# Kernel tuning notes

Measured on AMD Instinct MI355X. Metric: run time of the kernel, lower is better.

## Reference

```python
import jax, jax.numpy as jnp
import numpy as np

D_MODEL = 2048
B, T, N = 4, 2048, 512


def setup_inputs() -> dict:
    key = jax.random.key(0)
    k1, k2, k3, k4, k5 = jax.random.split(key, 5)
    x = jax.random.normal(k1, (B, T, D_MODEL), dtype=jnp.float32)
    h_stack = jax.random.normal(k2, (B, N, D_MODEL), dtype=jnp.float32)
    m_stack = jax.random.normal(k3, (B, N, D_MODEL), dtype=jnp.float32)
    m_current = jax.random.normal(k4, (B, T, D_MODEL), dtype=jnp.float32)
    # block-causal visibility: position t can see cache entry j iff j <= t*N/T
    causal_mask = jnp.arange(N)[None, :] <= (jnp.arange(T)[:, None] * N // T)
    # learned projection, torch Linear stores weight as (out, in): u = x @ W.T
    W_u = jax.random.normal(k5, (D_MODEL, D_MODEL), dtype=jnp.float32) * (1.0 / np.sqrt(D_MODEL))
    return {"x": x, "h_stack": h_stack, "m_stack": m_stack,
            "m_current": m_current, "causal_mask": causal_mask, "W_u": W_u}


def reference(x, h_stack, m_stack, m_current, causal_mask, W_u):
    D = x.shape[-1]
    n = m_stack.shape[1]
    scale = 1.0 / jnp.sqrt(jnp.asarray(D, x.dtype))
    u = jnp.einsum('btd,ed->bte', x, W_u)                      # Linear(no bias): x @ W.T
    scores_cached = jnp.einsum('btd,bnd->btn', u, m_stack) * scale
    neg_inf = jnp.asarray(-jnp.inf, scores_cached.dtype)
    scores_cached = jnp.where(causal_mask[None, :, :], scores_cached, neg_inf)
    scores_current = jnp.sum(u * m_current, axis=-1, keepdims=True) * scale  # (B,T,1)
    all_scores = jnp.concatenate([scores_cached, scores_current], axis=-1)   # (B,T,N+1)
    attn_weights = jax.nn.softmax(all_scores, axis=-1)
    gates_cached = attn_weights[:, :, :n]
    gate_current = attn_weights[:, :, n:]
    h_retrieved = jnp.einsum('btn,bnd->btd', gates_cached, h_stack)
    return h_retrieved, gate_current, attn_weights
```

## Files before the change

### kernel.cpp

```cpp
#include <hip/hip_runtime.h>

#define D_MODEL 2048
#define B_SZ 4
#define T_SZ 2048
#define N_SZ 512

typedef __bf16 bf16x8 __attribute__((ext_vector_type(8)));
typedef float f32x4 __attribute__((ext_vector_type(4)));
typedef ushort u16x8 __attribute__((ext_vector_type(8)));

__device__ __forceinline__ ushort f2bf(float f) {
  unsigned u = __float_as_uint(f);
  unsigned r = (u + 0x7fffu + ((u >> 16) & 1u)) >> 16;
  return (ushort)r;
}
__device__ __forceinline__ float bflo(unsigned w) { return __uint_as_float(w << 16); }
__device__ __forceinline__ float bfhi(unsigned w) { return __uint_as_float(w & 0xffff0000u); }

__device__ __forceinline__ void async_ld16(const ushort* g, ushort* l) {
  __builtin_amdgcn_global_load_lds(
      (const __attribute__((address_space(1))) void*)g,
      (__attribute__((address_space(3))) void*)l, 16, 0, 0);
}

__global__ __launch_bounds__(256) void conv_all(const float* __restrict__ x,
                                                const float* __restrict__ W,
                                                const float* __restrict__ ms,
                                                ushort* __restrict__ x_bf,
                                                ushort* __restrict__ W_bf,
                                                ushort* __restrict__ ms_bf) {
  const int bid = blockIdx.x;
  const float* src;
  ushort* dst;
  long blk;
  if (bid < 8192) { src = x; dst = x_bf; blk = bid; }
  else if (bid < 10240) { src = W; dst = W_bf; blk = bid - 8192; }
  else { src = ms; dst = ms_bf; blk = bid - 10240; }
  const long i = (blk * 256 + threadIdx.x) * 8;
  float4 a = *(const float4*)(src + i);
  float4 b = *(const float4*)(src + i + 4);
  u16x8 o;
  o[0] = f2bf(a.x); o[1] = f2bf(a.y); o[2] = f2bf(a.z); o[3] = f2bf(a.w);
  o[4] = f2bf(b.x); o[5] = f2bf(b.y); o[6] = f2bf(b.z); o[7] = f2bf(b.w);
  *(u16x8*)(dst + i) = o;
}

__global__ __launch_bounds__(256) void transpose_conv(const float* __restrict__ src,
                                                      ushort* __restrict__ dst) {
  __shared__ ushort tile[32][33];
  const int b = blockIdx.z;
  const int n0 = blockIdx.x * 32, d0 = blockIdx.y * 32;
  const int tx = threadIdx.x, ty = threadIdx.y;
  const float* s = src + (long)b * N_SZ * D_MODEL;
  ushort* d = dst + (long)b * D_MODEL * N_SZ;
#pragma unroll
  for (int r = 0; r < 4; r++)
    tile[ty + r * 8][tx] = f2bf(s[(long)(n0 + ty + r * 8) * D_MODEL + d0 + tx]);
  __syncthreads();
#pragma unroll
  for (int r = 0; r < 4; r++)
    d[(long)(d0 + ty + r * 8) * N_SZ + n0 + tx] = tile[tx][ty + r * 8];
}

template <int TM, int MASKMODE, bool OUT_BF16>
__global__ __launch_bounds__(256) void gemm_bt(const ushort* __restrict__ A,
                                               const ushort* __restrict__ Bt,
                                               void* __restrict__ Cv, int N, int K,
                                               long sA, long sB, long sC, float scale) {
  constexpr int NA = TM / 16;
  constexpr int NCH = NA + 8;
  constexpr int NC = NCH / 4;
  constexpr int NI = TM / 32;
  __shared__ __align__(16) ushort sa[TM * 32];
  __shared__ __align__(16) ushort sb[128 * 32];
  const int bz = blockIdx.z;
  const int row0 = blockIdx.y * TM;
  const int col0 = blockIdx.x * 128;
  if (MASKMODE == 1 && col0 > ((row0 + TM - 1) >> 2)) return;
  int Kend = K;
  if (MASKMODE == 2) {
    int kl = ((row0 + TM - 1) >> 2) + 1;
    Kend = min(K, (kl + 31) & ~31);
  }
  const ushort* Ab = A + (long)bz * sA;
  const ushort* Bb = Bt + (long)bz * sB;

  const int tid = threadIdx.x;
  const int w = tid >> 6, lane = tid & 63;
  const int wr = w >> 1, wc = w & 1;
  const int quad = lane >> 4, l16 = lane & 15;

  f32x4 acc[NI][4];
#pragma unroll
  for (int i = 0; i < NI; i++)
#pragma unroll
    for (int j = 0; j < 4; j++) acc[i][j] = (f32x4){0.f, 0.f, 0.f, 0.f};

  const int lrow = lane >> 2;
  const int lcol = (lane & 3) * 8;
  const ushort* gsrc[NC];
  ushort* ldst[NC];
#pragma unroll
  for (int t = 0; t < NC; t++) {
    const int c = w * NC + t;
    if (c < NA) {
      ldst[t] = sa + c * 512;
      gsrc[t] = Ab + (long)(row0 + c * 16 + lrow) * K + lcol;
    } else {
      ldst[t] = sb + (c - NA) * 512;
      gsrc[t] = Bb + (long)(col0 + (c - NA) * 16 + lrow) * K + lcol;
    }
  }

  for (int k0 = 0; k0 < Kend; k0 += 32) {
#pragma unroll
    for (int t = 0; t < NC; t++) async_ld16(gsrc[t] + k0, ldst[t]);
    __syncthreads();
    bf16x8 af[NI], bfr[4];
#pragma unroll
    for (int i = 0; i < NI; i++)
      af[i] = *(const bf16x8*)(sa + (wr * (TM / 2) + i * 16 + l16) * 32 + quad * 8);
#pragma unroll
    for (int j = 0; j < 4; j++)
      bfr[j] = *(const bf16x8*)(sb + (wc * 64 + j * 16 + l16) * 32 + quad * 8);
#pragma unroll
    for (int i = 0; i < NI; i++)
#pragma unroll
      for (int j = 0; j < 4; j++)
        acc[i][j] = __builtin_amdgcn_mfma_f32_16x16x32_bf16(af[i], bfr[j], acc[i][j], 0, 0, 0);
    __syncthreads();
  }

#pragma unroll
  for (int i = 0; i < NI; i++) {
    const int rb = row0 + wr * (TM / 2) + i * 16 + quad * 4;
#pragma unroll
    for (int j = 0; j < 4; j++) {
      const int c = col0 + wc * 64 + j * 16 + l16;
#pragma unroll
      for (int r = 0; r < 4; r++) {
        float v = acc[i][j][r] * scale;
        long off = (long)bz * sC + (long)(rb + r) * N + c;
        if (OUT_BF16)
          ((ushort*)Cv)[off] = f2bf(v);
        else
          ((float*)Cv)[off] = v;
      }
    }
  }
}

__global__ __launch_bounds__(256) void softmax_gate(const ushort* __restrict__ u_bf,
                                                    const float* __restrict__ m_cur,
                                                    const float* __restrict__ scores,
                                                    float* __restrict__ out_gc,
                                                    float* __restrict__ out_attn,
                                                    ushort* __restrict__ gates_bf) {
  const int wv = threadIdx.x >> 6, lane = threadIdx.x & 63;
  const int bt = blockIdx.x * 4 + wv;
  const int t = bt & (T_SZ - 1);
  const ushort* urow = u_bf + (long)bt * D_MODEL;
  const float* mrow = m_cur + (long)bt * D_MODEL;

  float part = 0.f;
#pragma unroll
  for (int c = 0; c < 4; c++) {
    uint4 uv = *(const uint4*)(urow + c * 512 + lane * 8);
    float4 m0 = *(const float4*)(mrow + c * 512 + lane * 8);
    float4 m1 = *(const float4*)(mrow + c * 512 + lane * 8 + 4);
    part += bflo(uv.x) * m0.x + bfhi(uv.x) * m0.y + bflo(uv.y) * m0.z + bfhi(uv.y) * m0.w +
            bflo(uv.z) * m1.x + bfhi(uv.z) * m1.y + bflo(uv.w) * m1.z + bfhi(uv.w) * m1.w;
  }
#pragma unroll
  for (int m = 32; m; m >>= 1) part += __shfl_xor(part, m, 64);
  const float curs = part * 0.022097086912079608f;

  const int nmax = t >> 2;
  const float* srow = scores + (long)bt * N_SZ;
  float sc[8];
  float lmax = curs;
#pragma unroll
  for (int k = 0; k < 8; k++) {
    const int n = k * 64 + lane;
    sc[k] = srow[n];
    if (n <= nmax) lmax = fmaxf(lmax, sc[k]);
  }
#pragma unroll
  for (int m = 32; m; m >>= 1) lmax = fmaxf(lmax, __shfl_xor(lmax, m, 64));

  float lsum = (lane == 0) ? __expf(curs - lmax) : 0.f;
#pragma unroll
  for (int k = 0; k < 8; k++) {
    const int n = k * 64 + lane;
    sc[k] = (n <= nmax) ? __expf(sc[k] - lmax) : 0.f;
    lsum += sc[k];
  }
#pragma unroll
  for (int m = 32; m; m >>= 1) lsum += __shfl_xor(lsum, m, 64);
  const float inv = 1.f / lsum;

  float* arow = out_attn + (long)bt * (N_SZ + 1);
  ushort* grow = gates_bf + (long)bt * N_SZ;
#pragma unroll
  for (int k = 0; k < 8; k++) {
    const int n = k * 64 + lane;
    const float wgt = sc[k] * inv;
    arow[n] = wgt;
    grow[n] = f2bf(wgt);
  }
  if (lane == 0) {
    const float g = __expf(curs - lmax) * inv;
    arow[N_SZ] = g;
    out_gc[bt] = g;
  }
}

extern "C" void kernel_launch(void* const* d_in, const int* in_sizes, int n_in,
                              void* d_out, int out_size, void* d_ws, size_t ws_size,
                              hipStream_t stream) {
  const float* x = (const float*)d_in[0];
  const float* h_stack = (const float*)d_in[1];
  const float* m_stack = (const float*)d_in[2];
  const float* m_cur = (const float*)d_in[3];
  const float* W = (const float*)d_in[5];

  float* out = (float*)d_out;
  float* out_h = out;
  float* out_gc = out + (long)B_SZ * T_SZ * D_MODEL;
  float* out_attn = out_gc + B_SZ * T_SZ;

  char* ws = (char*)d_ws;
  ushort* x_bf = (ushort*)ws;
  ushort* u_bf = x_bf + 16777216;
  ushort* W_bf = u_bf + 16777216;
  ushort* ms_bf = W_bf + 4194304;
  ushort* gates = ms_bf + 4194304;
  ushort* hsT = gates + 4194304;
  float* scores = (float*)(hsT + 4194304);

  conv_all<<<12288, 256, 0, stream>>>(x, W, m_stack, x_bf, W_bf, ms_bf);
  transpose_conv<<<dim3(N_SZ / 32, D_MODEL / 32, B_SZ), dim3(32, 8), 0, stream>>>(h_stack, hsT);

  gemm_bt<128, 0, true><<<dim3(D_MODEL / 128, (B_SZ * T_SZ) / 128, 1), 256, 0, stream>>>(
      x_bf, W_bf, u_bf, D_MODEL, D_MODEL, 0, 0, 0, 1.0f);

  gemm_bt<64, 1, false><<<dim3(N_SZ / 128, T_SZ / 64, B_SZ), 256, 0, stream>>>(
      u_bf, ms_bf, scores, N_SZ, D_MODEL, (long)T_SZ * D_MODEL, (long)N_SZ * D_MODEL,
      (long)T_SZ * N_SZ, 0.022097086912079608f);

  softmax_gate<<<(B_SZ * T_SZ) / 4, 256, 0, stream>>>(u_bf, m_cur, scores, out_gc, out_attn,
                                                      gates);

  gemm_bt<128, 2, false><<<dim3(D_MODEL / 128, T_SZ / 128, B_SZ), 256, 0, stream>>>(
      gates, hsT, out_h, D_MODEL, N_SZ, (long)T_SZ * N_SZ, (long)D_MODEL * N_SZ,
      (long)T_SZ * D_MODEL, 1.0f);
}
```

Before: 394.1 us.

## Add 256x256-tile 8-wave GEMM with phased prefetch for projection and retrieval

Adds a new GEMM kernel with 256x256 output tiles and 512 threads. It double-buffers LDS using async global-to-LDS loads split into four phases that interleave with MFMA bursts, and raises wave priority around the MFMA bursts. It replaces the 128-tile GEMM for both the x@W projection and the masked gates@h retrieval, aiming at more operand reuse per loaded byte and better overlap of loads with compute. The 128 KB of LDS per block allows only one block per CU, and the grids shrink to 256 blocks, so the load on each block is heavier and the register use is high.

```diff
diff --git a/kernel.cpp b/kernel.cpp
--- a/kernel.cpp
+++ b/kernel.cpp
@@ -150,6 +150,126 @@
   }
 }
 
+template <int MASKMODE, bool OUT_BF16>
+__global__ __launch_bounds__(512, 2) void gemm256(const ushort* __restrict__ A,
+                                                  const ushort* __restrict__ Bt,
+                                                  void* __restrict__ Cv, int N, int K,
+                                                  long sA, long sB, long sC, float scale) {
+  __shared__ __align__(16) ushort lds[2][2][256 * 64];
+  const int bz = blockIdx.z;
+  const int row0 = blockIdx.y * 256;
+  const int col0 = blockIdx.x * 256;
+  int Kend = K;
+  if (MASKMODE == 2) {
+    int kl = ((row0 + 255) >> 2) + 1;
+    Kend = min(K, (kl + 63) & ~63);
+  }
+  const int NT = Kend >> 6;
+  const ushort* Ab = A + (long)bz * sA;
+  const ushort* Bb = Bt + (long)bz * sB;
+
+  const int tid = threadIdx.x;
+  const int w = tid >> 6, lane = tid & 63;
+  const int wr = w >> 2, wc = w & 3;
+  const int quad = lane >> 4, l16 = lane & 15;
+
+  f32x4 acc[8][4];
+#pragma unroll
+  for (int i = 0; i < 8; i++)
+#pragma unroll
+    for (int j = 0; j < 4; j++) acc[i][j] = (f32x4){0.f, 0.f, 0.f, 0.f};
+
+  const int lrow = lane >> 3;
+  const int lcol = ((lane & 7) ^ lrow) << 3;
+  const ushort* gA[4];
+  const ushort* gB[4];
+#pragma unroll
+  for (int j = 0; j < 4; j++) {
+    gA[j] = Ab + (long)(row0 + j * 64 + w * 8 + lrow) * K + lcol;
+    gB[j] = Bb + (long)(col0 + j * 64 + w * 8 + lrow) * K + lcol;
+  }
+
+#define GPHASE(MQ, NQ)                                                                   \
+  do {                                                                                   \
+    bf16x8 af[4][2], bv[2][2];                                                           \
+    _Pragma("unroll") for (int m = 0; m < 4; m++) _Pragma("unroll")                      \
+        for (int ks = 0; ks < 2; ks++) {                                                 \
+      const int row = wr * 128 + MQ * 64 + m * 16 + l16;                                 \
+      af[m][ks] = *(const bf16x8*)&lds[cbuf][0]                                          \
+          [row * 64 + ((ks * 32 + quad * 8) ^ ((l16 & 7) << 3))];                        \
+    }                                                                                    \
+    _Pragma("unroll") for (int n = 0; n < 2; n++) _Pragma("unroll")                      \
+        for (int ks = 0; ks < 2; ks++) {                                                 \
+      const int row = wc * 64 + NQ * 32 + n * 16 + l16;                                  \
+      bv[n][ks] = *(const bf16x8*)&lds[cbuf][1]                                          \
+          [row * 64 + ((ks * 32 + quad * 8) ^ ((l16 & 7) << 3))];                        \
+    }                                                                                    \
+    __builtin_amdgcn_s_barrier();                                                        \
+    __builtin_amdgcn_s_setprio(1);                                                       \
+    _Pragma("unroll") for (int m = 0; m < 4; m++) _Pragma("unroll")                      \
+        for (int n = 0; n < 2; n++) _Pragma("unroll")                                    \
+            for (int ks = 0; ks < 2; ks++)                                               \
+      acc[MQ * 4 + m][NQ * 2 + n] = __builtin_amdgcn_mfma_f32_16x16x32_bf16(             \
+          af[m][ks], bv[n][ks], acc[MQ * 4 + m][NQ * 2 + n], 0, 0, 0);                   \
+    __builtin_amdgcn_s_setprio(0);                                                       \
+    __builtin_amdgcn_s_barrier();                                                        \
+  } while (0)
+
+#pragma unroll
+  for (int j = 0; j < 4; j++) {
+    async_ld16(gA[j], &lds[0][0][j * 4096 + w * 512]);
+    async_ld16(gB[j], &lds[0][1][j * 4096 + w * 512]);
+  }
+
+  for (int t = 0; t < NT; ++t) {
+    const int cbuf = t & 1;
+    const int kn = (t + 1) << 6;
+    if (t + 1 < NT) {
+      async_ld16(gA[0] + kn, &lds[cbuf ^ 1][0][0 * 4096 + w * 512]);
+      async_ld16(gB[0] + kn, &lds[cbuf ^ 1][1][0 * 4096 + w * 512]);
+      asm volatile("s_waitcnt vmcnt(2)" ::: "memory");
+    } else {
+      asm volatile("s_waitcnt vmcnt(0)" ::: "memory");
+    }
+    __builtin_amdgcn_s_barrier();
+    GPHASE(0, 0);
+    if (t + 1 < NT) {
+      async_ld16(gA[1] + kn, &lds[cbuf ^ 1][0][1 * 4096 + w * 512]);
+      async_ld16(gB[1] + kn, &lds[cbuf ^ 1][1][1 * 4096 + w * 512]);
+    }
+    GPHASE(0, 1);
+    if (t + 1 < NT) {
+      async_ld16(gA[2] + kn, &lds[cbuf ^ 1][0][2 * 4096 + w * 512]);
+      async_ld16(gB[2] + kn, &lds[cbuf ^ 1][1][2 * 4096 + w * 512]);
+    }
+    GPHASE(1, 0);
+    if (t + 1 < NT) {
+      async_ld16(gA[3] + kn, &lds[cbuf ^ 1][0][3 * 4096 + w * 512]);
+      async_ld16(gB[3] + kn, &lds[cbuf ^ 1][1][3 * 4096 + w * 512]);
+    }
+    GPHASE(1, 1);
+  }
+#undef GPHASE
+
+#pragma unroll
+  for (int i = 0; i < 8; i++) {
+    const int rb = row0 + wr * 128 + (i >> 2) * 64 + (i & 3) * 16 + quad * 4;
+#pragma unroll
+    for (int j = 0; j < 4; j++) {
+      const int cc = col0 + wc * 64 + (j >> 1) * 32 + (j & 1) * 16 + l16;
+#pragma unroll
+      for (int r = 0; r < 4; r++) {
+        float v = acc[i][j][r] * scale;
+        long off = (long)bz * sC + (long)(rb + r) * N + cc;
+        if (OUT_BF16)
+          ((ushort*)Cv)[off] = f2bf(v);
+        else
+          ((float*)Cv)[off] = v;
+      }
+    }
+  }
+}
+
 __global__ __launch_bounds__(256) void softmax_gate(const ushort* __restrict__ u_bf,
                                                     const float* __restrict__ m_cur,
                                                     const float* __restrict__ scores,
@@ -241,7 +361,7 @@
   conv_all<<<12288, 256, 0, stream>>>(x, W, m_stack, x_bf, W_bf, ms_bf);
   transpose_conv<<<dim3(N_SZ / 32, D_MODEL / 32, B_SZ), dim3(32, 8), 0, stream>>>(h_stack, hsT);
 
-  gemm_bt<128, 0, true><<<dim3(D_MODEL / 128, (B_SZ * T_SZ) / 128, 1), 256, 0, stream>>>(
+  gemm256<0, true><<<dim3(D_MODEL / 256, (B_SZ * T_SZ) / 256, 1), 512, 0, stream>>>(
       x_bf, W_bf, u_bf, D_MODEL, D_MODEL, 0, 0, 0, 1.0f);
 
   gemm_bt<64, 1, false><<<dim3(N_SZ / 128, T_SZ / 64, B_SZ), 256, 0, stream>>>(
@@ -251,7 +371,7 @@
   softmax_gate<<<(B_SZ * T_SZ) / 4, 256, 0, stream>>>(u_bf, m_cur, scores, out_gc, out_attn,
                                                       gates);
 
-  gemm_bt<128, 2, false><<<dim3(D_MODEL / 128, T_SZ / 128, B_SZ), 256, 0, stream>>>(
+  gemm256<2, false><<<dim3(D_MODEL / 256, T_SZ / 256, B_SZ), 512, 0, stream>>>(
       gates, hsT, out_h, D_MODEL, N_SZ, (long)T_SZ * N_SZ, (long)D_MODEL * N_SZ,
       (long)T_SZ * D_MODEL, 1.0f);
 }
```

Result: faster. 363.7 us (-7.7%).
